# Kernel tuning notes

Measured on AMD Instinct MI355X. Metric: run time of the kernel, lower is better.

The kernel has to match this reference:

```python
import jax, jax.numpy as jnp
import numpy as np

B, N, H = 16, 4096, 512
TANH_CLIP = 10.0
USE_TANH = True


def setup_inputs() -> dict:
    key = jax.random.key(0)
    k1, k2, k3, k4, k5 = jax.random.split(key, 5)
    stdv = 1.0 / np.sqrt(H)
    features = jax.random.normal(k1, (B, N, 2 * H), dtype=jnp.float32)
    query = jax.random.normal(k2, (B, 1, H), dtype=jnp.float32)
    Wf = jax.random.uniform(k3, (H, 2 * H), dtype=jnp.float32, minval=-stdv, maxval=stdv)
    Wq = jax.random.uniform(k4, (H, H), dtype=jnp.float32, minval=-stdv, maxval=stdv)
    v = jax.random.uniform(k5, (1, 1, H), dtype=jnp.float32, minval=-stdv, maxval=stdv)
    return {"features": features, "query": query, "Wf": Wf, "Wq": Wq, "v": v}


def reference(features, query, Wf, Wq, v):
    # projected_features: [B, N, H] = features [B,N,2H] @ Wf.T [2H,H]
    projected_features = jnp.einsum('bnf,hf->bnh', features, Wf)
    # projected_query: [B, 1, H]
    projected_query = jnp.einsum('bqf,hf->bqh', query, Wq)
    # fused add + tanh + weighted reduction over H with v -> u: [B, 1, N]
    hidden = jnp.tanh(projected_features + projected_query)  # [B, N, H]
    u = jnp.einsum('oih,bnh->bin', v, hidden)  # v [1,1,H] broadcast over batch -> [B,1,N]
    logits = TANH_CLIP * jnp.tanh(u) if USE_TANH else u
    return (projected_features, logits)
```

## Files before the change

kernel.cpp:

```cpp
#include <hip/hip_runtime.h>
#include <hip/hip_bf16.h>
#include <stdint.h>


#define KDIM 1024
#define HDIM 512

typedef short bf16x8 __attribute__((ext_vector_type(8)));
typedef float f32x4  __attribute__((ext_vector_type(4)));

__device__ __forceinline__ float fast_tanh(float x) {
    float ax = fabsf(x);
    float e  = __expf(-2.0f * ax);
    float r  = (1.0f - e) / (1.0f + e);
    return copysignf(r, x);
}

__device__ __forceinline__ short f2bf(float x) {
    __hip_bfloat16 b = __float2bfloat16(x);
    return (short)__builtin_bit_cast(unsigned short, b);
}

__device__ __forceinline__ bf16x8 cvt8(float4 a, float4 b) {
    bf16x8 o;
    o[0] = f2bf(a.x); o[1] = f2bf(a.y); o[2] = f2bf(a.z); o[3] = f2bf(a.w);
    o[4] = f2bf(b.x); o[5] = f2bf(b.y); o[6] = f2bf(b.z); o[7] = f2bf(b.w);
    return o;
}

__global__ void bshuf_kernel(const float* __restrict__ Wf, short* __restrict__ Bsh) {
    const int tid = blockIdx.x * 256 + threadIdx.x;
    const int kt  = tid >> 11;
    const int gg  = (tid >> 6) & 31;
    const int ln  = tid & 63;
    const int fm  = ln & 15, fkg = ln >> 4;
    const int col = gg * 16 + fm;
    const int k0  = kt * 32 + fkg * 8;
    const float* src = Wf + col * KDIM + k0;
    float4 a = *(const float4*)src;
    float4 b = *(const float4*)(src + 4);
    *(bf16x8*)(Bsh + (size_t)tid * 8) = cvt8(a, b);
}

__global__ void pq_kernel(const float* __restrict__ query,
                          const float* __restrict__ Wq,
                          float* __restrict__ pq) {
    const int t = blockIdx.x * blockDim.x + threadIdx.x;
    const int b = t >> 9, h = t & 511;
    const float4* q  = (const float4*)(query + (b << 9));
    const float4* wq = (const float4*)(Wq + ((size_t)h << 9));
    float s = 0.0f;
    #pragma unroll 4
    for (int i = 0; i < 128; ++i) {
        float4 a = q[i], c = wq[i];
        s += a.x * c.x + a.y * c.y + a.z * c.z + a.w * c.w;
    }
    pq[t] = s;
}

__global__ __launch_bounds__(256, 3) void gemm_kernel(
    const float* __restrict__ A, const short* __restrict__ Bsh,
    const float* __restrict__ pq, const float* __restrict__ v,
    float* __restrict__ pf, float* __restrict__ logits)
{
    __shared__ __align__(16) char ldsA[4][4096];
    __shared__ float uls[128];
    const int t    = threadIdx.x;
    const int lane = t & 63;
    const int w    = t >> 6;
    const int fm   = lane & 15;
    const int fkg  = lane >> 4;
    const int Mbase = blockIdx.x * 32;

    const int srow = t >> 3, sp = t & 7;
    const int asrc = srow * 4096 + ((sp ^ (srow & 7)) << 4);
    const int adst = t * 16;
    const char* Ab = (const char*)(A + (size_t)Mbase * KDIM);

    int ard[2][2];
    #pragma unroll
    for (int f = 0; f < 2; ++f) {
        const int r = f * 16 + fm;
        ard[f][0] = r * 128 + (((fkg * 2    ) ^ (r & 7)) << 4);
        ard[f][1] = r * 128 + (((fkg * 2 + 1) ^ (r & 7)) << 4);
    }

    const char* Bb = (const char*)Bsh + ((size_t)(w * 8 * 64) + lane) * 16;

    f32x4 acc[2][8];
    const f32x4 zf = {0.0f, 0.0f, 0.0f, 0.0f};
    #pragma unroll
    for (int f = 0; f < 2; ++f)
        #pragma unroll
        for (int g = 0; g < 8; ++g) acc[f][g] = zf;

    #define STAGE(BUF, KT) \
        __builtin_amdgcn_global_load_lds( \
            (const __attribute__((address_space(1))) void*)(Ab + asrc + ((KT) & 31) * 128), \
            (__attribute__((address_space(3))) void*)(&ldsA[BUF][adst]), 16, 0, 0)

    STAGE(0, 0);
    STAGE(1, 1);

    bf16x8 bfr[8], abf[2];

    #pragma unroll 2
    for (int kt = 0; kt < 32; ++kt) {
        const char* bk = Bb + (size_t)kt * 32768;
        #pragma unroll
        for (int g = 0; g < 8; ++g)
            bfr[g] = *(const bf16x8*)(bk + g * 1024);
        STAGE((kt + 2) & 3, kt + 2);
        asm volatile("s_waitcnt vmcnt(10)" ::: "memory");
        __builtin_amdgcn_s_barrier();
        asm volatile("" ::: "memory");
        const char* base = ldsA[kt & 3];
        #pragma unroll
        for (int f = 0; f < 2; ++f)
            abf[f] = cvt8(*(const float4*)(base + ard[f][0]),
                          *(const float4*)(base + ard[f][1]));
        #pragma unroll
        for (int f = 0; f < 2; ++f)
            #pragma unroll
            for (int g = 0; g < 8; ++g)
                acc[f][g] = __builtin_amdgcn_mfma_f32_16x16x32_bf16(
                    abf[f], bfr[g], acc[f][g], 0, 0, 0);
    }
    #undef STAGE

    const int bidx = Mbase >> 12;
    const float* pqb = pq + (bidx << 9);
    float vv[8], pv[8];
    #pragma unroll
    for (int g = 0; g < 8; ++g) {
        const int c = w * 128 + g * 16 + fm;
        vv[g] = v[c];
        pv[g] = pqb[c];
    }
    #pragma unroll
    for (int f = 0; f < 2; ++f) {
        #pragma unroll
        for (int rr = 0; rr < 4; ++rr) {
            const int rloc = f * 16 + fkg * 4 + rr;
            float* prow = pf + (size_t)(Mbase + rloc) * HDIM + w * 128 + fm;
            float s = 0.0f;
            #pragma unroll
            for (int g = 0; g < 8; ++g) {
                const float val = acc[f][g][rr];
                __builtin_nontemporal_store(val, &prow[g * 16]);
                s += vv[g] * fast_tanh(val + pv[g]);
            }
            s += __shfl_xor(s, 1);
            s += __shfl_xor(s, 2);
            s += __shfl_xor(s, 4);
            s += __shfl_xor(s, 8);
            if (fm == 0) uls[rloc * 4 + w] = s;
        }
    }
    __syncthreads();
    if (t < 32) {
        const float4 p4 = *(const float4*)(uls + t * 4);
        const float u = p4.x + p4.y + p4.z + p4.w;
        logits[Mbase + t] = 10.0f * fast_tanh(u);
    }
}

extern "C" void kernel_launch(void* const* d_in, const int* in_sizes, int n_in,
                              void* d_out, int out_size, void* d_ws, size_t ws_size,
                              hipStream_t stream) {
    const float* features = (const float*)d_in[0];
    const float* query    = (const float*)d_in[1];
    const float* Wf       = (const float*)d_in[2];
    const float* Wq       = (const float*)d_in[3];
    const float* v        = (const float*)d_in[4];

    float* pf     = (float*)d_out;
    float* logits = (float*)d_out + 33554432;

    float* ws_pq  = (float*)d_ws;
    short* ws_bsh = (short*)(ws_pq + 8192);

    bshuf_kernel<<<256, 256, 0, stream>>>(Wf, ws_bsh);
    pq_kernel<<<16, 512, 0, stream>>>(query, Wq, ws_pq);
    gemm_kernel<<<2048, 256, 0, stream>>>(features, ws_bsh, ws_pq, v, pf, logits);
}
```

Measured before the change: 191.8 us.

## Deepen GEMM pipeline with register double-buffered B and 3-ahead A staging

The GEMM main loop now stages A tiles into LDS three steps ahead instead of two. B fragments are double-buffered in registers and loaded two iterations ahead, issued after each step's MFMAs. The vmcnt waits are retuned to match, and the MFMA block is wrapped in s_setprio to favor the math wave. The goal is to hide global-load latency for both operands. In exchange it uses more VGPRs for the second B register set and issues a few redundant wrapped loads at the tail.

```diff
diff --git a/kernel.cpp b/kernel.cpp
--- a/kernel.cpp
+++ b/kernel.cpp
@@ -74,7 +74,6 @@
 
     const int srow = t >> 3, sp = t & 7;
     const int asrc = srow * 4096 + ((sp ^ (srow & 7)) << 4);
-    const int adst = t * 16;
     const char* Ab = (const char*)(A + (size_t)Mbase * KDIM);
 
     int ard[2][2];
@@ -85,7 +84,7 @@
         ard[f][1] = r * 128 + (((fkg * 2 + 1) ^ (r & 7)) << 4);
     }
 
-    const char* Bb = (const char*)Bsh + ((size_t)(w * 8 * 64) + lane) * 16;
+    const char* Bb = (const char*)Bsh + (size_t)(w * 8 * 64 + lane) * 16;
 
     f32x4 acc[2][8];
     const f32x4 zf = {0.0f, 0.0f, 0.0f, 0.0f};
@@ -94,39 +93,61 @@
         #pragma unroll
         for (int g = 0; g < 8; ++g) acc[f][g] = zf;
 
-    #define STAGE(BUF, KT) \
+    bf16x8 b0[8], b1[8];
+
+    #define STAGE(SLOT, KS) \
         __builtin_amdgcn_global_load_lds( \
-            (const __attribute__((address_space(1))) void*)(Ab + asrc + ((KT) & 31) * 128), \
-            (__attribute__((address_space(3))) void*)(&ldsA[BUF][adst]), 16, 0, 0)
+            (const __attribute__((address_space(1))) void*)(Ab + asrc + ((KS) & 31) * 128), \
+            (__attribute__((address_space(3))) void*)(&ldsA[SLOT][t * 16]), 16, 0, 0)
+
+    #define LOADB(SET, KT) do {                                              \
+        const char* bk_ = Bb + (size_t)((KT) & 31) * 32768;                  \
+        _Pragma("unroll")                                                    \
+        for (int g = 0; g < 8; ++g)                                          \
+            SET[g] = *(const bf16x8*)(bk_ + g * 1024);                       \
+    } while (0)
+
+    #define STEP(KT, BC, WAITN) do {                                         \
+        asm volatile("s_waitcnt vmcnt(" #WAITN ")" ::: "memory");            \
+        __builtin_amdgcn_s_barrier();                                        \
+        asm volatile("" ::: "memory");                                       \
+        STAGE(((KT) + 3) & 3, (KT) + 3);                                     \
+        const char* base = ldsA[(KT) & 3];                                   \
+        float4 ra0 = *(const float4*)(base + ard[0][0]);                     \
+        float4 ra1 = *(const float4*)(base + ard[0][1]);                     \
+        float4 ra2 = *(const float4*)(base + ard[1][0]);                     \
+        float4 ra3 = *(const float4*)(base + ard[1][1]);                     \
+        bf16x8 a0 = cvt8(ra0, ra1);                                          \
+        bf16x8 a1 = cvt8(ra2, ra3);                                          \
+        __builtin_amdgcn_s_setprio(1);                                       \
+        _Pragma("unroll")                                                    \
+        for (int g = 0; g < 8; ++g)                                          \
+            acc[0][g] = __builtin_amdgcn_mfma_f32_16x16x32_bf16(             \
+                a0, BC[g], acc[0][g], 0, 0, 0);                              \
+        _Pragma("unroll")                                                    \
+        for (int g = 0; g < 8; ++g)                                          \
+            acc[1][g] = __builtin_amdgcn_mfma_f32_16x16x32_bf16(             \
+                a1, BC[g], acc[1][g], 0, 0, 0);                              \
+        __builtin_amdgcn_s_setprio(0);                                       \
+        LOADB(BC, (KT) + 2);                                                 \
+    } while (0)
 
     STAGE(0, 0);
     STAGE(1, 1);
-
-    bf16x8 bfr[8], abf[2];
-
-    #pragma unroll 2
-    for (int kt = 0; kt < 32; ++kt) {
-        const char* bk = Bb + (size_t)kt * 32768;
-        #pragma unroll
-        for (int g = 0; g < 8; ++g)
-            bfr[g] = *(const bf16x8*)(bk + g * 1024);
-        STAGE((kt + 2) & 3, kt + 2);
-        asm volatile("s_waitcnt vmcnt(10)" ::: "memory");
-        __builtin_amdgcn_s_barrier();
-        asm volatile("" ::: "memory");
-        const char* base = ldsA[kt & 3];
-        #pragma unroll
-        for (int f = 0; f < 2; ++f)
-            abf[f] = cvt8(*(const float4*)(base + ard[f][0]),
-                          *(const float4*)(base + ard[f][1]));
-        #pragma unroll
-        for (int f = 0; f < 2; ++f)
-            #pragma unroll
-            for (int g = 0; g < 8; ++g)
-                acc[f][g] = __builtin_amdgcn_mfma_f32_16x16x32_bf16(
-                    abf[f], bfr[g], acc[f][g], 0, 0, 0);
-    }
+    STAGE(2, 2);
+    LOADB(b0, 0);
+    LOADB(b1, 1);
+
+    STEP(0, b0, 8);
+    #pragma unroll 1
+    for (int kt2 = 0; kt2 < 15; ++kt2) {
+        STEP(2 * kt2 + 1, b1, 9);
+        STEP(2 * kt2 + 2, b0, 9);
+    }
+    STEP(31, b1, 9);
+    #undef STEP
     #undef STAGE
+    #undef LOADB
 
     const int bidx = Mbase >> 12;
     const float* pqb = pq + (bidx << 9);
```

Result: no change. 190.9 us (-0.5%).
